# Kernel optimization log

Measured on AMD Instinct MI355X. Metric: run time of the kernel, lower is better.

## Reference

```python
import jax, jax.numpy as jnp
import numpy as np

B, U, V, H, K = 256, 4096, 80, 1024, 10

def setup_inputs() -> dict:
    key = jax.random.key(0)
    ks = jax.random.split(key, 6)
    return {
        "x": jax.random.normal(ks[0], (B, 1, H), dtype=jnp.float32),
        "c": jax.random.normal(ks[1], (B, U, V), dtype=jnp.float32),
        "kappa": jax.random.uniform(ks[2], (B, K), dtype=jnp.float32),
        "W": jax.random.normal(ks[3], (3 * K, H), dtype=jnp.float32) * 0.02,
        "b": jax.random.normal(ks[4], (3 * K,), dtype=jnp.float32) * 0.02,
        "ascii_lengths": jax.random.randint(ks[5], (B,), 0, U, dtype=jnp.int64),
    }

def reference(x, c, kappa, W, b, ascii_lengths):
    # x: [B,1,H], c: [B,U,V], kappa: [B,K]
    Bu, Uu = c.shape[0], c.shape[1]
    lin = x[:, 0, :] @ W.T + b                      # [B,3K]
    alpha_hat, beta_hat, kappa_hat = jnp.split(lin, 3, axis=-1)
    alpha = jnp.exp(alpha_hat)                      # [B,K]
    beta = jnp.exp(beta_hat)                        # [B,K]
    new_kappa = kappa + jnp.exp(kappa_hat - 3.9)    # [B,K]
    u = jnp.arange(Uu + 1, dtype=x.dtype)[None, :, None]          # [1,U+1,1]
    phi_components = alpha[:, None, :] * jnp.exp(
        -beta[:, None, :] * (new_kappa[:, None, :] - u) ** 2)     # [B,U+1,K]
    phi_termination = phi_components.sum(axis=-1)[:, None, :]     # [B,1,U+1]
    phi = phi_termination[:, :, :-1]                              # [B,1,U]
    mask = (jnp.arange(Uu)[None, :] < ascii_lengths[:, None])[:, None, :]  # [B,1,U]
    phi = jnp.where(mask, phi, jnp.zeros((), dtype=phi.dtype))
    w = jnp.einsum('bqu,buv->bqv', phi, c)          # [B,1,V]
    return w, new_kappa, phi_termination
```

## Files before the change

kernel.cpp:

```cpp
#include <hip/hip_runtime.h>
#include <math.h>

#define B_SZ 256
#define U_SZ 4096
#define V_SZ 80
#define H_SZ 1024
#define K_SZ 10
#define CPRE 64
#define CPRE_F4 (CPRE * V_SZ / 4)

#define OUT_W_OFF      0
#define OUT_NK_OFF     (B_SZ * V_SZ)
#define OUT_PT_OFF     (B_SZ * V_SZ + B_SZ * K_SZ)

__global__ __launch_bounds__(1024) void fused_softwindow(
        const float* __restrict__ x,
        const float* __restrict__ c,
        const float* __restrict__ kappa,
        const float* __restrict__ W,
        const float* __restrict__ bias,
        const int*   __restrict__ lens,
        float* __restrict__ out) {
    __shared__ float cs[CPRE * V_SZ];
    __shared__ float lin_s[32];
    __shared__ float a_s[K_SZ], nb_s[K_SZ], nk_s[K_SZ];
    __shared__ float phi_s[U_SZ];
    __shared__ float wpart[12][V_SZ];
    __shared__ int   ucut_sh;

    const int b    = blockIdx.x;
    const int tid  = threadIdx.x;
    const int wave = tid >> 6;
    const int lane = tid & 63;
    const int len  = lens[b];

    const float*  cb  = c + (size_t)b * U_SZ * V_SZ;
    const float4* cb4 = (const float4*)cb;

    float4 creg0, creg1;
    creg0 = cb4[tid];
    if (tid < CPRE_F4 - 1024) creg1 = cb4[tid + 1024];

    float kap = 0.f, bs0 = 0.f, bs1 = 0.f, bs2 = 0.f;
    if (tid < K_SZ) {
        kap = kappa[b * K_SZ + tid];
        bs0 = bias[tid];
        bs1 = bias[K_SZ + tid];
        bs2 = bias[2 * K_SZ + tid];
    }

    #pragma unroll
    for (int i = tid; i < U_SZ; i += 1024) phi_s[i] = 0.f;

    {
        const float4* xb4 = (const float4*)(x + (size_t)b * H_SZ);
        float4 xv[4];
        #pragma unroll
        for (int j = 0; j < 4; ++j) xv[j] = xb4[lane + 64 * j];
        for (int k = wave; k < 3 * K_SZ; k += 16) {
            const float4* Wk4 = (const float4*)(W + (size_t)k * H_SZ);
            float p = 0.f;
            #pragma unroll
            for (int j = 0; j < 4; ++j) {
                float4 wv = Wk4[lane + 64 * j];
                p += wv.x * xv[j].x + wv.y * xv[j].y +
                     wv.z * xv[j].z + wv.w * xv[j].w;
            }
            #pragma unroll
            for (int off = 32; off > 0; off >>= 1) p += __shfl_down(p, off);
            if (lane == 0) lin_s[k] = p;
        }
    }

    float* pt = out + OUT_PT_OFF + (size_t)b * (U_SZ + 1);
    for (int u = CPRE + tid; u <= U_SZ; u += 1024) pt[u] = 0.f;

    __syncthreads();

    {
        float4* cs4 = (float4*)cs;
        cs4[tid] = creg0;
        if (tid < CPRE_F4 - 1024) cs4[tid + 1024] = creg1;
    }

    if (wave == 0) {
        float cut = 0.f;
        if (lane < K_SZ) {
            const int k = lane;
            float ah = lin_s[k]            + bs0;
            float bh = lin_s[K_SZ + k]     + bs1;
            float kh = lin_s[2 * K_SZ + k] + bs2;
            float alpha = expf(ah);
            float beta  = expf(bh);
            float nk    = kap + expf(kh - 3.9f);
            a_s[k]  = alpha;
            nb_s[k] = -beta;
            nk_s[k] = nk;
            cut = nk + sqrtf((60.f + fmaxf(ah, 0.f)) / beta);
            out[OUT_NK_OFF + b * K_SZ + k] = nk;
        }
        #pragma unroll
        for (int off = 8; off > 0; off >>= 1)
            cut = fmaxf(cut, __shfl_xor(cut, off));
        if (lane == 0) {
            int uc = (int)cut + 1;
            ucut_sh = uc > U_SZ ? U_SZ : uc;
        }
    }
    __syncthreads();

    const int ucut = ucut_sh;

    for (int u = tid; u <= ucut; u += 1024) {
        const float fu = (float)u;
        float s = 0.f;
        #pragma unroll
        for (int k = 0; k < K_SZ; ++k) {
            float d = nk_s[k] - fu;
            s += a_s[k] * expf(nb_s[k] * d * d);
        }
        pt[u] = s;
        if (u < len && u < U_SZ) phi_s[u] = s;
    }
    for (int u = ucut + 1 + tid; u < CPRE; u += 1024) pt[u] = 0.f;

    __syncthreads();

    const int ulim = min(min(len, ucut + 1), U_SZ);
    if (tid < 12 * V_SZ) {
        const int v = tid % V_SZ;
        const int r = tid / V_SZ;
        float acc = 0.f;
        #pragma unroll
        for (int j = 0; j < 6; ++j) {
            const int u = r + 12 * j;
            if (u < CPRE) acc += phi_s[u] * cs[u * V_SZ + v];
        }
        if (ulim > CPRE) {
            int u0 = r + ((CPRE - r + 11) / 12) * 12;
            for (int u = u0; u < ulim; u += 12)
                acc += phi_s[u] * cb[(size_t)u * V_SZ + v];
        }
        wpart[r][v] = acc;
    }
    __syncthreads();
    if (tid < V_SZ) {
        float s = 0.f;
        #pragma unroll
        for (int r = 0; r < 12; ++r) s += wpart[r][tid];
        out[OUT_W_OFF + b * V_SZ + tid] = s;
    }
}

extern "C" void kernel_launch(void* const* d_in, const int* in_sizes, int n_in,
                              void* d_out, int out_size, void* d_ws, size_t ws_size,
                              hipStream_t stream) {
    const float* x     = (const float*)d_in[0];
    const float* c     = (const float*)d_in[1];
    const float* kappa = (const float*)d_in[2];
    const float* W     = (const float*)d_in[3];
    const float* bias  = (const float*)d_in[4];
    const int*   lens  = (const int*)d_in[5];
    float* out = (float*)d_out;

    fused_softwindow<<<B_SZ, 1024, 0, stream>>>(x, c, kappa, W, bias, lens, out);
}
```

Baseline: 11.79 us.

## Compute phi redundantly per thread, drop shared phi/c staging and extra barriers

Every thread now derives alpha, beta and new_kappa for all K components itself from lin_s, so the single-wave parameter stage and its barrier go away. The w-reduction threads recompute phi inline for each u and read c straight from global memory, which removes the shared phi and c staging buffers and one more barrier. The leftover 64 threads write phi_termination and new_kappa. The c prefetch is kept only as an asm-pinned warm-up load whose values are never used. This trades redundant exp work per thread for fewer synchronisations and less shared-memory traffic.

After: 16.42 us. +39.3%, slower.

```diff
diff --git a/kernel.cpp b/kernel.cpp
--- a/kernel.cpp
+++ b/kernel.cpp
@@ -7,7 +7,6 @@
 #define H_SZ 1024
 #define K_SZ 10
 #define CPRE 64
-#define CPRE_F4 (CPRE * V_SZ / 4)
 
 #define OUT_W_OFF      0
 #define OUT_NK_OFF     (B_SZ * V_SZ)
@@ -21,12 +20,8 @@
         const float* __restrict__ bias,
         const int*   __restrict__ lens,
         float* __restrict__ out) {
-    __shared__ float cs[CPRE * V_SZ];
     __shared__ float lin_s[32];
-    __shared__ float a_s[K_SZ], nb_s[K_SZ], nk_s[K_SZ];
-    __shared__ float phi_s[U_SZ];
     __shared__ float wpart[12][V_SZ];
-    __shared__ int   ucut_sh;
 
     const int b    = blockIdx.x;
     const int tid  = threadIdx.x;
@@ -37,113 +32,96 @@
     const float*  cb  = c + (size_t)b * U_SZ * V_SZ;
     const float4* cb4 = (const float4*)cb;
 
-    float4 creg0, creg1;
-    creg0 = cb4[tid];
-    if (tid < CPRE_F4 - 1024) creg1 = cb4[tid + 1024];
+    float4 cw0 = cb4[tid];
+    float4 cw1 = cb4[tid + 1024];
 
-    float kap = 0.f, bs0 = 0.f, bs1 = 0.f, bs2 = 0.f;
-    if (tid < K_SZ) {
-        kap = kappa[b * K_SZ + tid];
-        bs0 = bias[tid];
-        bs1 = bias[K_SZ + tid];
-        bs2 = bias[2 * K_SZ + tid];
+    const float4* xb4 = (const float4*)(x + (size_t)b * H_SZ);
+    float4 xv[4];
+    #pragma unroll
+    for (int j = 0; j < 4; ++j) xv[j] = xb4[lane + 64 * j];
+
+    float* pt = out + OUT_PT_OFF + (size_t)b * (U_SZ + 1);
+    #pragma unroll
+    for (int j = 0; j < 4; ++j) {
+        int u = CPRE + tid + 1024 * j;
+        if (u <= U_SZ) pt[u] = 0.f;
     }
 
+    for (int k = wave; k < 3 * K_SZ; k += 16) {
+        const float4* Wk4 = (const float4*)(W + (size_t)k * H_SZ);
+        float p = 0.f;
+        #pragma unroll
+        for (int j = 0; j < 4; ++j) {
+            float4 wv = Wk4[lane + 64 * j];
+            p += wv.x * xv[j].x + wv.y * xv[j].y +
+                 wv.z * xv[j].z + wv.w * xv[j].w;
+        }
+        #pragma unroll
+        for (int off = 32; off > 0; off >>= 1) p += __shfl_down(p, off);
+        if (lane == 0) lin_s[k] = p;
+    }
+
+    asm volatile("" :: "v"(cw0.x), "v"(cw0.y), "v"(cw0.z), "v"(cw0.w),
+                       "v"(cw1.x), "v"(cw1.y), "v"(cw1.z), "v"(cw1.w));
+
+    __syncthreads();
+
+    float a_[K_SZ], nb_[K_SZ], nk_[K_SZ];
+    float cut = 0.f;
     #pragma unroll
-    for (int i = tid; i < U_SZ; i += 1024) phi_s[i] = 0.f;
+    for (int k = 0; k < K_SZ; ++k) {
+        float ah = lin_s[k]             + bias[k];
+        float bh = lin_s[K_SZ + k]      + bias[K_SZ + k];
+        float kh = lin_s[2 * K_SZ + k]  + bias[2 * K_SZ + k];
+        float al = expf(ah);
+        float bt = expf(bh);
+        float nkv = kappa[b * K_SZ + k] + expf(kh - 3.9f);
+        a_[k]  = al;
+        nb_[k] = -bt;
+        nk_[k] = nkv;
+        cut = fmaxf(cut, nkv + sqrtf((60.f + fmaxf(ah, 0.f)) / bt));
+    }
+    int ucut = (int)cut + 1;
+    if (ucut > U_SZ) ucut = U_SZ;
 
-    {
-        const float4* xb4 = (const float4*)(x + (size_t)b * H_SZ);
-        float4 xv[4];
-        #pragma unroll
-        for (int j = 0; j < 4; ++j) xv[j] = xb4[lane + 64 * j];
-        for (int k = wave; k < 3 * K_SZ; k += 16) {
-            const float4* Wk4 = (const float4*)(W + (size_t)k * H_SZ);
-            float p = 0.f;
+    if (tid < 12 * V_SZ) {
+        const int v = tid % V_SZ;
+        const int r = tid / V_SZ;
+        const int ulim = min(len, ucut + 1);
+        float acc = 0.f;
+        for (int u = r; u < ulim; u += 12) {
+            const float fu = (float)u;
+            float s = 0.f;
             #pragma unroll
-            for (int j = 0; j < 4; ++j) {
-                float4 wv = Wk4[lane + 64 * j];
-                p += wv.x * xv[j].x + wv.y * xv[j].y +
-                     wv.z * xv[j].z + wv.w * xv[j].w;
+            for (int k = 0; k < K_SZ; ++k) {
+                float d = nk_[k] - fu;
+                s += a_[k] * expf(nb_[k] * d * d);
             }
+            acc += s * cb[(size_t)u * V_SZ + v];
+        }
+        wpart[r][v] = acc;
+    } else {
+        const int t = tid - 12 * V_SZ;
+        for (int u = t; u <= ucut; u += 64) {
+            const float fu = (float)u;
+            float s = 0.f;
             #pragma unroll
-            for (int off = 32; off > 0; off >>= 1) p += __shfl_down(p, off);
-            if (lane == 0) lin_s[k] = p;
+            for (int k = 0; k < K_SZ; ++k) {
+                float d = nk_[k] - fu;
+                s += a_[k] * expf(nb_[k] * d * d);
+            }
+            pt[u] = s;
+        }
+        for (int u = ucut + 1 + t; u < CPRE; u += 64) pt[u] = 0.f;
+        if (t < K_SZ) {
+            float kh = lin_s[2 * K_SZ + t] + bias[2 * K_SZ + t];
+            out[OUT_NK_OFF + b * K_SZ + t] =
+                kappa[b * K_SZ + t] + expf(kh - 3.9f);
         }
     }
 
-    float* pt = out + OUT_PT_OFF + (size_t)b * (U_SZ + 1);
-    for (int u = CPRE + tid; u <= U_SZ; u += 1024) pt[u] = 0.f;
-
     __syncthreads();
 
-    {
-        float4* cs4 = (float4*)cs;
-        cs4[tid] = creg0;
-        if (tid < CPRE_F4 - 1024) cs4[tid + 1024] = creg1;
-    }
-
-    if (wave == 0) {
-        float cut = 0.f;
-        if (lane < K_SZ) {
-            const int k = lane;
-            float ah = lin_s[k]            + bs0;
-            float bh = lin_s[K_SZ + k]     + bs1;
-            float kh = lin_s[2 * K_SZ + k] + bs2;
-            float alpha = expf(ah);
-            float beta  = expf(bh);
-            float nk    = kap + expf(kh - 3.9f);
-            a_s[k]  = alpha;
-            nb_s[k] = -beta;
-            nk_s[k] = nk;
-            cut = nk + sqrtf((60.f + fmaxf(ah, 0.f)) / beta);
-            out[OUT_NK_OFF + b * K_SZ + k] = nk;
-        }
-        #pragma unroll
-        for (int off = 8; off > 0; off >>= 1)
-            cut = fmaxf(cut, __shfl_xor(cut, off));
-        if (lane == 0) {
-            int uc = (int)cut + 1;
-            ucut_sh = uc > U_SZ ? U_SZ : uc;
-        }
-    }
-    __syncthreads();
-
-    const int ucut = ucut_sh;
-
-    for (int u = tid; u <= ucut; u += 1024) {
-        const float fu = (float)u;
-        float s = 0.f;
-        #pragma unroll
-        for (int k = 0; k < K_SZ; ++k) {
-            float d = nk_s[k] - fu;
-            s += a_s[k] * expf(nb_s[k] * d * d);
-        }
-        pt[u] = s;
-        if (u < len && u < U_SZ) phi_s[u] = s;
-    }
-    for (int u = ucut + 1 + tid; u < CPRE; u += 1024) pt[u] = 0.f;
-
-    __syncthreads();
-
-    const int ulim = min(min(len, ucut + 1), U_SZ);
-    if (tid < 12 * V_SZ) {
-        const int v = tid % V_SZ;
-        const int r = tid / V_SZ;
-        float acc = 0.f;
-        #pragma unroll
-        for (int j = 0; j < 6; ++j) {
-            const int u = r + 12 * j;
-            if (u < CPRE) acc += phi_s[u] * cs[u * V_SZ + v];
-        }
-        if (ulim > CPRE) {
-            int u0 = r + ((CPRE - r + 11) / 12) * 12;
-            for (int u = u0; u < ulim; u += 12)
-                acc += phi_s[u] * cb[(size_t)u * V_SZ + v];
-        }
-        wpart[r][v] = acc;
-    }
-    __syncthreads();
     if (tid < V_SZ) {
         float s = 0.f;
         #pragma unroll
```
